# Performance work log

Hardware: AMD Instinct MI355X
Metric: run time of the kernel (lower is better)

## Reference

```python
import jax, jax.numpy as jnp
import numpy as np

B, C, H, W = 4, 128, 64, 64
CQ = C // 8  # query/key channels = 16


def setup_inputs() -> dict:
    key = jax.random.key(0)
    ks = jax.random.split(key, 8)
    s = 0.05
    return {
        "x": jax.random.normal(ks[0], (B, C, H, W), jnp.float32),
        "wq": jax.random.normal(ks[1], (CQ, C), jnp.float32) * s,
        "bq": jax.random.normal(ks[2], (CQ,), jnp.float32) * s,
        "wk": jax.random.normal(ks[3], (CQ, C), jnp.float32) * s,
        "bk": jax.random.normal(ks[4], (CQ,), jnp.float32) * s,
        "wv": jax.random.normal(ks[5], (C, C), jnp.float32) * s,
        "bv": jax.random.normal(ks[6], (C,), jnp.float32) * s,
        # original inits gamma to 0; use small nonzero so attention path is exercised
        "gamma": jax.random.normal(ks[7], (1,), jnp.float32) * 0.1,
    }


def reference(x, wq, bq, wk, bk, wv, bv, gamma):
    b, c, h, w = x.shape
    n = h * w
    xf = x.reshape(b, c, n)  # [B, C, N]
    # 1x1 convs are per-position linear maps over channels
    q = jnp.einsum("qc,bcn->bnq", wq, xf) + bq            # [B, N, Cq]
    k = jnp.einsum("qc,bcn->bqn", wk, xf) + bk[:, None]   # [B, Cq, N]
    v = jnp.einsum("oc,bcn->bon", wv, xf) + bv[:, None]   # [B, C, N]
    # unscaled scores, softmax over keys (last dim), as in the original
    attn = jax.nn.softmax(jnp.einsum("bnq,bqm->bnm", q, k), axis=-1)  # [B, N, N]
    # out = value @ attention^T : out[b,c,n] = sum_m v[b,c,m] * attn[b,n,m]
    out = jnp.einsum("bom,bnm->bon", v, attn)             # [B, C, N]
    return gamma[0] * out.reshape(b, c, h, w) + x
```

## Files before the change

### kernel.cpp

```cpp
#include <hip/hip_runtime.h>
#include <hip/hip_bf16.h>

typedef float f32x4  __attribute__((ext_vector_type(4)));
typedef float f32x16 __attribute__((ext_vector_type(16)));
typedef short s16x8  __attribute__((ext_vector_type(8)));

#define NB 4
#define NC 128
#define NNPOS 4096
#define KSP 8
#define LOG2E 1.44269504088896f

__device__ __forceinline__ short bf16s(float x) {
    __hip_bfloat16 h = __float2bfloat16(x);
    return *reinterpret_cast<short*>(&h);
}
__device__ __forceinline__ int packbf2(float lo, float hi) {
    __hip_bfloat162 t = __float22bfloat162_rn(float2{lo, hi});
    return *reinterpret_cast<int*>(&t);
}
__device__ __forceinline__ float bf2f(unsigned short u) {
    unsigned int v = ((unsigned int)u) << 16;
    return *reinterpret_cast<float*>(&v);
}
__device__ __forceinline__ float exp2fast(float x) {
    return __builtin_amdgcn_exp2f(x);
}

__global__ __launch_bounds__(256) void qkv_kernel(
    const float* __restrict__ x,
    const float* __restrict__ wq, const float* __restrict__ bq,
    const float* __restrict__ wk, const float* __restrict__ bk,
    const float* __restrict__ wv, const float* __restrict__ bv,
    short* __restrict__ qb, short* __restrict__ kb, short* __restrict__ vt)
{
    const int n0  = blockIdx.x * 32;
    const int b   = blockIdx.y;
    const int tid = threadIdx.x;
    const int w = tid >> 6, lane = tid & 63, quad = lane >> 4, nn = lane & 15;

    __shared__ __align__(16) short xsT[32 * 136];

    #pragma unroll
    for (int p = 0; p < 4; ++p) {
        int idx = tid + p * 256;
        int cc = idx >> 3, n4 = (idx & 7) * 4;
        f32x4 xv = *(const f32x4*)&x[((size_t)(b * NC + cc)) * NNPOS + n0 + n4];
        #pragma unroll
        for (int j = 0; j < 4; ++j)
            xsT[(n4 + j) * 136 + cc] = bf16s(xv[j]);
    }

    s16x8 af[3][4];
    bool  live[3];
    f32x4 biasv[3];
    #pragma unroll
    for (int t = 0; t < 3; ++t) {
        int rid = 3 * w + t;
        int R   = rid * 16;
        const float* wsrc = nullptr; const float* bsrc = nullptr; int row0 = 0;
        float scale = 1.0f;
        if (rid < 8)        { wsrc = wv; bsrc = bv; row0 = R; }
        else if (rid == 8)  { wsrc = wq; bsrc = bq; row0 = 0; scale = LOG2E; }
        else if (rid == 10) { wsrc = wk; bsrc = bk; row0 = 0; }
        live[t] = (wsrc != nullptr);
        #pragma unroll
        for (int r = 0; r < 4; ++r)
            biasv[t][r] = live[t] ? scale * bsrc[row0 + quad * 4 + r] : 0.0f;
        if (live[t]) {
            #pragma unroll
            for (int ks = 0; ks < 4; ++ks) {
                const float* src = wsrc + (size_t)(row0 + nn) * NC + ks * 32 + quad * 8;
                f32x4 wa = *(const f32x4*)src;
                f32x4 wb = *(const f32x4*)(src + 4);
                s16x8 f;
                #pragma unroll
                for (int j = 0; j < 4; ++j) {
                    f[j]     = bf16s(scale * wa[j]);
                    f[j + 4] = bf16s(scale * wb[j]);
                }
                af[t][ks] = f;
            }
        }
    }
    __syncthreads();

    f32x4 acc[3][2];
    #pragma unroll
    for (int t = 0; t < 3; ++t)
        #pragma unroll
        for (int nt = 0; nt < 2; ++nt)
            acc[t][nt] = biasv[t];

    #pragma unroll
    for (int nt = 0; nt < 2; ++nt) {
        s16x8 bf[4];
        #pragma unroll
        for (int ks = 0; ks < 4; ++ks)
            bf[ks] = *(const s16x8*)&xsT[(nt * 16 + nn) * 136 + ks * 32 + quad * 8];
        #pragma unroll
        for (int t = 0; t < 3; ++t)
            if (live[t])
                #pragma unroll
                for (int ks = 0; ks < 4; ++ks)
                    acc[t][nt] = __builtin_amdgcn_mfma_f32_16x16x32_bf16(af[t][ks], bf[ks], acc[t][nt], 0, 0, 0);
    }

    const int slot = (nn & 3) | ((nn & 4) << 1) | ((nn & 8) >> 1);

    #pragma unroll
    for (int t = 0; t < 3; ++t) {
        if (!live[t]) continue;
        int R = (3 * w + t) * 16;
        #pragma unroll
        for (int nt = 0; nt < 2; ++nt) {
            int n = n0 + nt * 16 + nn;
            int kg = (n0 + nt * 16) >> 4;
            #pragma unroll
            for (int r = 0; r < 4; ++r) {
                short v = bf16s(acc[t][nt][r]);
                int row = R + quad * 4 + r;
                if (row < 128) {
                    int ct = row >> 5, c31r = row & 31;
                    vt[((((size_t)b * 256 + kg) * 4 + ct) * 32 + c31r) * 16 + slot] = v;
                } else if (row < 144)
                    qb[((size_t)(b * NNPOS) + n) * 16 + (row - 128)] = v;
                else
                    kb[((size_t)(b * NNPOS) + n) * 16 + (row - 160)] = v;
            }
        }
    }
}

__global__ __launch_bounds__(256, 3) void attn_kernel(
    const short* __restrict__ qb, const short* __restrict__ kb,
    const short* __restrict__ vt,
    unsigned short* __restrict__ Ow, float* __restrict__ lw)
{
    const int s   = blockIdx.x;
    const int b   = blockIdx.z;
    const int tid = threadIdx.x;
    const int w = tid >> 6, lane = tid & 63, h = lane >> 5, c31 = lane & 31;

    const int q0 = (blockIdx.y * 4 + w) * 32;

    s16x8 bq = *(const s16x8*)(qb + ((size_t)(b * NNPOS) + q0 + c31) * 16 + h * 8);

    f32x16 acc[4];
    #pragma unroll
    for (int ct = 0; ct < 4; ++ct)
        #pragma unroll
        for (int r = 0; r < 16; ++r) acc[ct][r] = 0.0f;
    float lp0 = 0.f, lp1 = 0.f;

    const short* kbp = kb + (size_t)(b * NNPOS) * 16;
    const short* vbp = vt + (size_t)b * (256 * 4 * 512);
    const int mbase = s * (NNPOS / KSP);
    const int kgbase = mbase >> 4;
    const int voff = (c31 << 4) + (h << 3);

    for (int it = 0; it < (NNPOS / KSP) / 64; ++it) {
        const int m0 = mbase + it * 64;
        const int kg0 = kgbase + it * 4;

        s16x8 ak0 = *(const s16x8*)(kbp + (size_t)(m0      + c31) * 16 + h * 8);
        s16x8 ak1 = *(const s16x8*)(kbp + (size_t)(m0 + 32 + c31) * 16 + h * 8);
        s16x8 vb01[2][4];
        #pragma unroll
        for (int p = 0; p < 2; ++p)
            #pragma unroll
            for (int ct = 0; ct < 4; ++ct)
                vb01[p][ct] = *(const s16x8*)(vbp +
                    (((size_t)(kg0 + p) * 4 + ct) << 9) + voff);

        f32x16 z;
        #pragma unroll
        for (int r = 0; r < 16; ++r) z[r] = 0.0f;
        f32x16 s0 = __builtin_amdgcn_mfma_f32_32x32x16_bf16(ak0, bq, z, 0, 0, 0);
        f32x16 s1 = __builtin_amdgcn_mfma_f32_32x32x16_bf16(ak1, bq, z, 0, 0, 0);

        s16x8 pa[4];
        #pragma unroll
        for (int p = 0; p < 4; ++p) {
            const f32x16& sv = (p < 2) ? s0 : s1;
            const int off = (p & 1) * 8;
            union { int i[4]; s16x8 v; } u;
            #pragma unroll
            for (int j = 0; j < 4; ++j) {
                float p0 = exp2fast(sv[off + 2 * j]);
                float p1 = exp2fast(sv[off + 2 * j + 1]);
                if (j & 1) lp1 += p0 + p1; else lp0 += p0 + p1;
                u.i[j] = packbf2(p0, p1);
            }
            pa[p] = u.v;
        }

        #pragma unroll
        for (int p = 0; p < 2; ++p)
            #pragma unroll
            for (int ct = 0; ct < 4; ++ct)
                acc[ct] = __builtin_amdgcn_mfma_f32_32x32x16_bf16(
                    pa[p], vb01[p][ct], acc[ct], 0, 0, 0);

        s16x8 vb23[2][4];
        #pragma unroll
        for (int p = 0; p < 2; ++p)
            #pragma unroll
            for (int ct = 0; ct < 4; ++ct)
                vb23[p][ct] = *(const s16x8*)(vbp +
                    (((size_t)(kg0 + 2 + p) * 4 + ct) << 9) + voff);
        #pragma unroll
        for (int p = 0; p < 2; ++p)
            #pragma unroll
            for (int ct = 0; ct < 4; ++ct)
                acc[ct] = __builtin_amdgcn_mfma_f32_32x32x16_bf16(
                    pa[2 + p], vb23[p][ct], acc[ct], 0, 0, 0);
    }

    float lp = lp0 + lp1;
    lp += __shfl_xor(lp, 32, 64);
    if (lane < 32)
        lw[((size_t)(b * KSP + s)) * NNPOS + q0 + c31] = lp;

    #pragma unroll
    for (int ct = 0; ct < 4; ++ct)
        #pragma unroll
        for (int r = 0; r < 16; ++r) {
            int q = q0 + (r & 3) + 8 * (r >> 2) + 4 * h;
            Ow[(((size_t)(b * KSP + s)) * NNPOS + q) * NC + ct * 32 + c31] =
                (unsigned short)bf16s(acc[ct][r]);
        }
}

__global__ __launch_bounds__(256) void combine_kernel(
    const unsigned short* __restrict__ Ow, const float* __restrict__ lw,
    const float* __restrict__ x, const float* __restrict__ gamma,
    float* __restrict__ out)
{
    const int n0  = blockIdx.x * 64;
    const int b   = blockIdx.y;
    const int tid = threadIdx.x;

    __shared__ float ot[128 * 65 + 64];
    float* lsum = ot + 128 * 65;

    if (tid < 64) {
        float sl = 0.f;
        #pragma unroll
        for (int sI = 0; sI < KSP; ++sI)
            sl += lw[((size_t)(b * KSP + sI)) * NNPOS + n0 + tid];
        lsum[tid] = sl;
    }
    __syncthreads();

    #pragma unroll
    for (int p = 0; p < 8; ++p) {
        int e = tid + p * 256;
        int cq = e & 31, n = e >> 5;
        float a0 = 0.f, a1 = 0.f, a2 = 0.f, a3 = 0.f;
        #pragma unroll
        for (int sI = 0; sI < KSP; ++sI) {
            const unsigned short* src = Ow +
                (((size_t)(b * KSP + sI)) * NNPOS + n0 + n) * NC + cq * 4;
            ushort4 u = *(const ushort4*)src;
            a0 += bf2f(u.x); a1 += bf2f(u.y); a2 += bf2f(u.z); a3 += bf2f(u.w);
        }
        float inv = 1.0f / lsum[n];
        ot[(cq * 4) * 65 + n]     = a0 * inv;
        ot[(cq * 4 + 1) * 65 + n] = a1 * inv;
        ot[(cq * 4 + 2) * 65 + n] = a2 * inv;
        ot[(cq * 4 + 3) * 65 + n] = a3 * inv;
    }
    __syncthreads();

    const float g = gamma[0];
    #pragma unroll
    for (int p = 0; p < 32; ++p) {
        int e = tid + p * 256;
        int n = e & 63, c = e >> 6;
        size_t a = ((size_t)(b * NC + c)) * NNPOS + n0 + n;
        out[a] = g * ot[c * 65 + n] + x[a];
    }
}

extern "C" void kernel_launch(void* const* d_in, const int* in_sizes, int n_in,
                              void* d_out, int out_size, void* d_ws, size_t ws_size,
                              hipStream_t stream) {
    const float* x     = (const float*)d_in[0];
    const float* wq    = (const float*)d_in[1];
    const float* bq    = (const float*)d_in[2];
    const float* wk    = (const float*)d_in[3];
    const float* bk    = (const float*)d_in[4];
    const float* wv    = (const float*)d_in[5];
    const float* bv    = (const float*)d_in[6];
    const float* gamma = (const float*)d_in[7];
    float* out = (float*)d_out;

    short* qb = (short*)d_ws;
    short* kb = qb + (size_t)NB * NNPOS * 16;
    short* vt = kb + (size_t)NB * NNPOS * 16;
    unsigned short* Ow = (unsigned short*)(vt + (size_t)NB * NC * NNPOS);
    float* lw = (float*)(Ow + (size_t)NB * KSP * NNPOS * NC);

    qkv_kernel<<<dim3(128, NB), 256, 0, stream>>>(x, wq, bq, wk, bk, wv, bv, qb, kb, vt);
    attn_kernel<<<dim3(KSP, 32, NB), 256, 0, stream>>>(qb, kb, vt, Ow, lw);
    combine_kernel<<<dim3(NNPOS / 64, NB), 256, 0, stream>>>(Ow, lw, x, gamma, out);
}
```

Measured before the change: 115.8 us.

## Rebalance key splits, stage V stores via LDS, prefetch K, vectorize combine

Reduces the key-split count from 8 to 6 with uneven 11/10-iteration chunks, which changes the grid size and the partial-output traffic. The QKV kernel now stages V in shared memory and writes it out with coalesced 16-byte stores, and writes q/k as packed short4 instead of scattered scalar stores. The attention loop prefetches the next K fragments and raises wave priority around the MFMA blocks. The combine kernel uses 16-byte bf16 loads, a precomputed reciprocal and float4 output and residual accesses. These are several independent changes, and fewer splits may lower occupancy across the attention grid.

```diff
diff --git a/kernel.cpp b/kernel.cpp
--- a/kernel.cpp
+++ b/kernel.cpp
@@ -8,7 +8,7 @@
 #define NB 4
 #define NC 128
 #define NNPOS 4096
-#define KSP 8
+#define KSP 6
 #define LOG2E 1.44269504088896f
 
 __device__ __forceinline__ short bf16s(float x) {
@@ -40,6 +40,7 @@
     const int w = tid >> 6, lane = tid & 63, quad = lane >> 4, nn = lane & 15;
 
     __shared__ __align__(16) short xsT[32 * 136];
+    __shared__ __align__(16) short vstage[4096];
 
     #pragma unroll
     for (int p = 0; p < 4; ++p) {
@@ -111,23 +112,37 @@
     #pragma unroll
     for (int t = 0; t < 3; ++t) {
         if (!live[t]) continue;
-        int R = (3 * w + t) * 16;
+        const int rid = 3 * w + t;
         #pragma unroll
         for (int nt = 0; nt < 2; ++nt) {
-            int n = n0 + nt * 16 + nn;
-            int kg = (n0 + nt * 16) >> 4;
-            #pragma unroll
-            for (int r = 0; r < 4; ++r) {
-                short v = bf16s(acc[t][nt][r]);
-                int row = R + quad * 4 + r;
-                if (row < 128) {
-                    int ct = row >> 5, c31r = row & 31;
-                    vt[((((size_t)b * 256 + kg) * 4 + ct) * 32 + c31r) * 16 + slot] = v;
-                } else if (row < 144)
-                    qb[((size_t)(b * NNPOS) + n) * 16 + (row - 128)] = v;
-                else
-                    kb[((size_t)(b * NNPOS) + n) * 16 + (row - 160)] = v;
+            if (rid < 8) {
+                #pragma unroll
+                for (int r = 0; r < 4; ++r) {
+                    int row = rid * 16 + quad * 4 + r;
+                    vstage[(((nt << 2) | (row >> 5)) << 9) + ((row & 31) << 4) + slot]
+                        = bf16s(acc[t][nt][r]);
+                }
+            } else {
+                short4 pk;
+                pk.x = bf16s(acc[t][nt][0]);
+                pk.y = bf16s(acc[t][nt][1]);
+                pk.z = bf16s(acc[t][nt][2]);
+                pk.w = bf16s(acc[t][nt][3]);
+                int n = n0 + nt * 16 + nn;
+                short* dst = (rid == 8 ? qb : kb) +
+                             ((size_t)(b * NNPOS) + n) * 16 + quad * 4;
+                *reinterpret_cast<short4*>(dst) = pk;
             }
+        }
+    }
+    __syncthreads();
+
+    {
+        short* vdst = vt + ((size_t)(b * 256) + (n0 >> 4)) * 2048;
+        #pragma unroll
+        for (int p = 0; p < 2; ++p) {
+            int off = (tid + p * 256) * 8;
+            *(s16x8*)&vdst[off] = *(const s16x8*)&vstage[off];
         }
     }
 }
@@ -155,16 +170,22 @@
 
     const short* kbp = kb + (size_t)(b * NNPOS) * 16;
     const short* vbp = vt + (size_t)b * (256 * 4 * 512);
-    const int mbase = s * (NNPOS / KSP);
+    const int nit    = (s < 4) ? 11 : 10;
+    const int mbase  = (s < 4) ? s * 704 : 2816 + (s - 4) * 640;
     const int kgbase = mbase >> 4;
     const int voff = (c31 << 4) + (h << 3);
 
-    for (int it = 0; it < (NNPOS / KSP) / 64; ++it) {
-        const int m0 = mbase + it * 64;
+    f32x16 z;
+    #pragma unroll
+    for (int r = 0; r < 16; ++r) z[r] = 0.0f;
+
+    int m0 = mbase;
+    s16x8 ak0 = *(const s16x8*)(kbp + (size_t)(m0      + c31) * 16 + h * 8);
+    s16x8 ak1 = *(const s16x8*)(kbp + (size_t)(m0 + 32 + c31) * 16 + h * 8);
+
+    for (int it = 0; it < nit; ++it) {
         const int kg0 = kgbase + it * 4;
 
-        s16x8 ak0 = *(const s16x8*)(kbp + (size_t)(m0      + c31) * 16 + h * 8);
-        s16x8 ak1 = *(const s16x8*)(kbp + (size_t)(m0 + 32 + c31) * 16 + h * 8);
         s16x8 vb01[2][4];
         #pragma unroll
         for (int p = 0; p < 2; ++p)
@@ -173,11 +194,14 @@
                 vb01[p][ct] = *(const s16x8*)(vbp +
                     (((size_t)(kg0 + p) * 4 + ct) << 9) + voff);
 
-        f32x16 z;
-        #pragma unroll
-        for (int r = 0; r < 16; ++r) z[r] = 0.0f;
         f32x16 s0 = __builtin_amdgcn_mfma_f32_32x32x16_bf16(ak0, bq, z, 0, 0, 0);
         f32x16 s1 = __builtin_amdgcn_mfma_f32_32x32x16_bf16(ak1, bq, z, 0, 0, 0);
+
+        if (it + 1 < nit) {
+            m0 += 64;
+            ak0 = *(const s16x8*)(kbp + (size_t)(m0      + c31) * 16 + h * 8);
+            ak1 = *(const s16x8*)(kbp + (size_t)(m0 + 32 + c31) * 16 + h * 8);
+        }
 
         s16x8 pa[4];
         #pragma unroll
@@ -195,12 +219,14 @@
             pa[p] = u.v;
         }
 
+        __builtin_amdgcn_s_setprio(1);
         #pragma unroll
         for (int p = 0; p < 2; ++p)
             #pragma unroll
             for (int ct = 0; ct < 4; ++ct)
                 acc[ct] = __builtin_amdgcn_mfma_f32_32x32x16_bf16(
                     pa[p], vb01[p][ct], acc[ct], 0, 0, 0);
+        __builtin_amdgcn_s_setprio(0);
 
         s16x8 vb23[2][4];
         #pragma unroll
@@ -209,12 +235,15 @@
             for (int ct = 0; ct < 4; ++ct)
                 vb23[p][ct] = *(const s16x8*)(vbp +
                     (((size_t)(kg0 + 2 + p) * 4 + ct) << 9) + voff);
+
+        __builtin_amdgcn_s_setprio(1);
         #pragma unroll
         for (int p = 0; p < 2; ++p)
             #pragma unroll
             for (int ct = 0; ct < 4; ++ct)
                 acc[ct] = __builtin_amdgcn_mfma_f32_32x32x16_bf16(
                     pa[2 + p], vb23[p][ct], acc[ct], 0, 0, 0);
+        __builtin_amdgcn_s_setprio(0);
     }
 
     float lp = lp0 + lp1;
@@ -249,37 +278,44 @@
         #pragma unroll
         for (int sI = 0; sI < KSP; ++sI)
             sl += lw[((size_t)(b * KSP + sI)) * NNPOS + n0 + tid];
-        lsum[tid] = sl;
+        lsum[tid] = 1.0f / sl;
     }
     __syncthreads();
 
+    #pragma unroll
+    for (int p = 0; p < 4; ++p) {
+        int e = tid + p * 256;
+        int co = e & 15, n = e >> 4;
+        float a[8] = {0.f, 0.f, 0.f, 0.f, 0.f, 0.f, 0.f, 0.f};
+        #pragma unroll
+        for (int sI = 0; sI < KSP; ++sI) {
+            const unsigned short* src = Ow +
+                (((size_t)(b * KSP + sI)) * NNPOS + n0 + n) * NC + co * 8;
+            union { s16x8 v; unsigned short us[8]; } u;
+            u.v = *(const s16x8*)src;
+            #pragma unroll
+            for (int j = 0; j < 8; ++j) a[j] += bf2f(u.us[j]);
+        }
+        float inv = lsum[n];
+        #pragma unroll
+        for (int j = 0; j < 8; ++j)
+            ot[(co * 8 + j) * 65 + n] = a[j] * inv;
+    }
+    __syncthreads();
+
+    const float g = gamma[0];
     #pragma unroll
     for (int p = 0; p < 8; ++p) {
         int e = tid + p * 256;
-        int cq = e & 31, n = e >> 5;
-        float a0 = 0.f, a1 = 0.f, a2 = 0.f, a3 = 0.f;
-        #pragma unroll
-        for (int sI = 0; sI < KSP; ++sI) {
-            const unsigned short* src = Ow +
-                (((size_t)(b * KSP + sI)) * NNPOS + n0 + n) * NC + cq * 4;
-            ushort4 u = *(const ushort4*)src;
-            a0 += bf2f(u.x); a1 += bf2f(u.y); a2 += bf2f(u.z); a3 += bf2f(u.w);
-        }
-        float inv = 1.0f / lsum[n];
-        ot[(cq * 4) * 65 + n]     = a0 * inv;
-        ot[(cq * 4 + 1) * 65 + n] = a1 * inv;
-        ot[(cq * 4 + 2) * 65 + n] = a2 * inv;
-        ot[(cq * 4 + 3) * 65 + n] = a3 * inv;
-    }
-    __syncthreads();
-
-    const float g = gamma[0];
-    #pragma unroll
-    for (int p = 0; p < 32; ++p) {
-        int e = tid + p * 256;
-        int n = e & 63, c = e >> 6;
-        size_t a = ((size_t)(b * NC + c)) * NNPOS + n0 + n;
-        out[a] = g * ot[c * 65 + n] + x[a];
+        int nq = e & 15, c = e >> 4;
+        size_t a = ((size_t)(b * NC + c)) * NNPOS + n0 + nq * 4;
+        float4 xv = *(const float4*)&x[a];
+        float4 o;
+        o.x = g * ot[c * 65 + nq * 4]     + xv.x;
+        o.y = g * ot[c * 65 + nq * 4 + 1] + xv.y;
+        o.z = g * ot[c * 65 + nq * 4 + 2] + xv.z;
+        o.w = g * ot[c * 65 + nq * 4 + 3] + xv.w;
+        *(float4*)&out[a] = o;
     }
 }
 
```

Result: slower. 119.8 us (+3.4%).
